# Optimization experiments

Hardware: AMD Instinct MI355X
Metric: run time of the kernel (lower is better)

Reference implementation:

```python
import jax, jax.numpy as jnp
import numpy as np

K = 49        # k_neighbors
EPS = 1e-5    # BatchNorm2d eps


def setup_inputs() -> dict:
    key = jax.random.key(0)
    ks = jax.random.split(key, 2)
    B, C, M, O = 64, 64, 32, 128
    X = jax.random.normal(ks[0], (B, C, M, M), dtype=jnp.float32)
    # conv1x1 weight (kaiming fan_out) flattened to (O, C); bias init 0
    W = jax.random.normal(ks[1], (O, C), dtype=jnp.float32) * (2.0 / O) ** 0.5
    b = jnp.zeros((O,), jnp.float32)
    gamma = jnp.ones((O,), jnp.float32)
    beta = jnp.zeros((O,), jnp.float32)
    run_mean = jnp.zeros((O,), jnp.float32)
    run_var = jnp.ones((O,), jnp.float32)
    return dict(X=X, W=W, b=b, gamma=gamma, beta=beta,
                run_mean=run_mean, run_var=run_var)


def _knn_aggregate(x):
    """x: (N, C) node features -> D^{-1/2} A D^{-1/2} x for the kNN graph."""
    N = x.shape[0]
    sq = jnp.sum(x * x, axis=1)
    d2 = sq[:, None] + sq[None, :] - 2.0 * (x @ x.T)
    dist = jnp.sqrt(jnp.maximum(d2, 0.0))              # torch.cdist (p=2)
    i = jnp.arange(N)
    dist = dist.at[i, i].set(jnp.inf)                  # fill_diagonal_(inf)
    _, knn = jax.lax.top_k(-dist, K)                   # (N, K) nearest indices
    # topk indices are distinct -> every row degree == K, and the column
    # normalizer uses the col node's row degree (also K), so
    # D^{-1/2} A D^{-1/2} x == mean of gathered neighbors.
    nb = x[knn]                                        # (N, K, C) gather
    return nb.sum(axis=1) / K


def reference(X, W, b, gamma, beta, run_mean, run_var):
    B, C, M, _ = X.shape
    N = M * M
    x = X.reshape(B, C, N).transpose(0, 2, 1)          # (B, N, C) nodes
    Z = jax.vmap(_knn_aggregate)(x)                    # (B, N, C) sparse GCN agg
    # 1x1 conv over the (M, M) grid == per-node linear map
    Fg = jnp.einsum('oc,bnc->bon', W, Z) + b[None, :, None]   # (B, O, N)
    Fg = jax.nn.relu(Fg)
    # BatchNorm2d with running stats (eval mode); Dropout2d is identity in eval
    inv = jax.lax.rsqrt(run_var + EPS)
    Fg = gamma[None, :, None] * (Fg - run_mean[None, :, None]) * inv[None, :, None] + beta[None, :, None]
    return Fg.mean(axis=2)                             # AdaptiveAvgPool2d(1) -> (B, O)
```

## Files before the change

kernel.cpp:

```cpp
#include <hip/hip_runtime.h>
#include <stdint.h>

#define BATCH 64
#define CDIM  64
#define NPTS  1024
#define ODIM  128
#define KNN   49
#define KNNP  52
#define BNEPS 1e-5f

typedef __attribute__((ext_vector_type(8))) short bf16x8;
typedef __attribute__((ext_vector_type(4))) float f32x4;

__device__ __forceinline__ int mbcnt64(unsigned long long m) {
    return __builtin_amdgcn_mbcnt_hi((uint32_t)(m >> 32),
           __builtin_amdgcn_mbcnt_lo((uint32_t)m, 0));
}

#define O_XF   0
#define SZ_XF  (BATCH*64*2*64*8*4)
#define O_SQ   (O_XF + SZ_XF)
#define SZ_SQ  (BATCH*NPTS*4)
#define O_KNN  (O_SQ + SZ_SQ)
#define SZ_KNN (BATCH*NPTS*KNNP*4)
#define O_Z    (O_KNN + SZ_KNN)
#define SZ_Z   (BATCH*NPTS*CDIM*4)
#define WS_NEED ((size_t)(O_Z + SZ_Z))

__global__ void gcn_init(const float* __restrict__ gamma, const float* __restrict__ beta,
                         const float* __restrict__ rmean, const float* __restrict__ rvar,
                         float* __restrict__ out) {
    int i = blockIdx.x * 256 + threadIdx.x;
    if (i < BATCH * ODIM) {
        int o = i & (ODIM - 1);
        out[i] = beta[o] - gamma[o] * rmean[o] * rsqrtf(rvar[o] + BNEPS);
    }
}

__global__ __launch_bounds__(256) void k0_split(const float* __restrict__ X,
                                                uint32_t* __restrict__ XF,
                                                float* __restrict__ sq,
                                                const float* __restrict__ gamma,
                                                const float* __restrict__ beta,
                                                const float* __restrict__ rmean,
                                                const float* __restrict__ rvar,
                                                float* __restrict__ out) {
    if (blockIdx.x < 32) {
        int i = blockIdx.x * 256 + threadIdx.x;
        int o = i & (ODIM - 1);
        out[i] = beta[o] - gamma[o] * rmean[o] * rsqrtf(rvar[o] + BNEPS);
    }
    const int b    = blockIdx.x >> 4;
    const int t16  = (blockIdx.x & 15) * 4 + (threadIdx.x >> 6);
    const int lane = threadIdx.x & 63;
    const int n    = t16 * 16 + (lane & 15);
    const int cg   = lane >> 4;
    const float* Xb = X + (size_t)b * CDIM * NPTS;
    float s = 0.f;
    for (int ks = 0; ks < 2; ks++) {
        uint32_t hi[4], lo[4];
#pragma unroll
        for (int dj = 0; dj < 4; dj++) {
            uint32_t hw[2], lw[2];
#pragma unroll
            for (int e = 0; e < 2; e++) {
                int c = ks * 32 + cg * 8 + dj * 2 + e;
                float x = Xb[(size_t)c * NPTS + n];
                s += x * x;
                uint32_t u  = __float_as_uint(x);
                uint32_t hr = (u + 0x7FFFu + ((u >> 16) & 1u)) >> 16;
                float    hf = __uint_as_float(hr << 16);
                uint32_t ul = __float_as_uint(x - hf);
                uint32_t lr = (ul + 0x7FFFu + ((ul >> 16) & 1u)) >> 16;
                hw[e] = hr; lw[e] = lr;
            }
            hi[dj] = hw[0] | (hw[1] << 16);
            lo[dj] = lw[0] | (lw[1] << 16);
        }
        size_t entry = ((size_t)(b * 64 + t16) * 2 + ks) * 64 + lane;
        uint32_t* p = XF + entry * 8;
        *(uint4*)p       = make_uint4(hi[0], hi[1], hi[2], hi[3]);
        *(uint4*)(p + 4) = make_uint4(lo[0], lo[1], lo[2], lo[3]);
    }
    s += __shfl_xor(s, 16, 64);
    s += __shfl_xor(s, 32, 64);
    if (lane < 16) sq[b * NPTS + n] = s;
}

__global__ __launch_bounds__(512, 6) void k1_gram_select(const uint32_t* __restrict__ XF,
                                                         const float* __restrict__ sq,
                                                         int* __restrict__ knn) {
    __shared__ uint32_t s_pk[8 * 1024];
    const int b    = blockIdx.x >> 6;
    const int rt   = blockIdx.x & 63;
    const int wave = threadIdx.x >> 6, lane = threadIdx.x & 63;
    const int q = lane >> 4, l15 = lane & 15;

    bf16x8 ahi[2], alo[2];
#pragma unroll
    for (int ks = 0; ks < 2; ks++) {
        const uint32_t* p = XF + (((size_t)(b * 64 + rt) * 2 + ks) * 64 + lane) * 8;
        ahi[ks] = *(const bf16x8*)p;
        alo[ks] = *(const bf16x8*)(p + 4);
    }
    const float* sqb = sq + b * NPTS;

#pragma unroll
    for (int tt = 0; tt < 8; tt++) {
        const int t16 = wave * 8 + tt;
        f32x4 acc = {0.f, 0.f, 0.f, 0.f};
#pragma unroll
        for (int ks = 0; ks < 2; ks++) {
            const uint32_t* p = XF + (((size_t)(b * 64 + t16) * 2 + ks) * 64 + lane) * 8;
            bf16x8 bhi = *(const bf16x8*)p;
            bf16x8 blo = *(const bf16x8*)(p + 4);
            acc = __builtin_amdgcn_mfma_f32_16x16x32_bf16(ahi[ks], bhi, acc, 0, 0, 0);
            acc = __builtin_amdgcn_mfma_f32_16x16x32_bf16(alo[ks], bhi, acc, 0, 0, 0);
            acc = __builtin_amdgcn_mfma_f32_16x16x32_bf16(ahi[ks], blo, acc, 0, 0, 0);
        }
        const int col  = t16 * 16 + l15;
        const float sqv = sqb[col];
        uint32_t k16[4];
#pragma unroll
        for (int i = 0; i < 4; i++) {
            int row = q * 4 + i;
            float d = fmaf(-2.f, acc[i], sqv);
            if (col == rt * 16 + row) d = __uint_as_float(0x7F800000u);
            uint32_t u = __float_as_uint(d);
            uint32_t key = ((int)u < 0) ? ~u : (u | 0x80000000u);
            k16[i] = key >> 16;
        }
        const int p0 = 2 * q, p1 = 2 * q + 1;
        s_pk[p0 * 1024 + (col ^ ((p0 & 3) << 3))] = k16[0] | (k16[1] << 16);
        s_pk[p1 * 1024 + (col ^ ((p1 & 3) << 3))] = k16[2] | (k16[3] << 16);
    }
    __syncthreads();

    uint32_t k0r[16], k1r[16];
    {
        const int sw = (wave & 3) << 3;
#pragma unroll
        for (int tt = 0; tt < 16; tt++) {
            uint32_t pk = s_pk[wave * 1024 + ((tt * 64 + lane) ^ sw)];
            k0r[tt] = pk & 0xFFFFu;
            k1r[tt] = pk >> 16;
        }
    }

    uint32_t lo0, hi0, lo1, hi1;
    {
        uint32_t lm0 = k0r[0], lm1 = k1r[0];
#pragma unroll
        for (int tt = 1; tt < 16; tt++) {
            lm0 = k0r[tt] < lm0 ? k0r[tt] : lm0;
            lm1 = k1r[tt] < lm1 ? k1r[tt] : lm1;
        }
        uint32_t g0 = lm0, m0 = lm0, g1 = lm1, m1 = lm1;
#pragma unroll
        for (int off = 1; off < 64; off <<= 1) {
            uint32_t a0 = (uint32_t)__shfl_xor((int)g0, off, 64);
            uint32_t b0 = (uint32_t)__shfl_xor((int)m0, off, 64);
            uint32_t a1 = (uint32_t)__shfl_xor((int)g1, off, 64);
            uint32_t b1 = (uint32_t)__shfl_xor((int)m1, off, 64);
            g0 = a0 < g0 ? a0 : g0;  m0 = b0 > m0 ? b0 : m0;
            g1 = a1 < g1 ? a1 : g1;  m1 = b1 > m1 ? b1 : m1;
        }
        lo0 = g0; hi0 = m0;
        lo1 = g1; hi1 = m1;
    }

    for (int it = 0; it < 16; it++) {
        bool a0 = lo0 < hi0, a1 = lo1 < hi1;
        if (!a0 && !a1) break;
        uint32_t mid0 = (lo0 + hi0) >> 1;
        uint32_t mid1 = (lo1 + hi1) >> 1;
        int cnt0 = 0, cnt1 = 0;
#pragma unroll
        for (int tt = 0; tt < 16; tt++) {
            cnt0 += __popcll(__ballot(k0r[tt] <= mid0));
            cnt1 += __popcll(__ballot(k1r[tt] <= mid1));
        }
        if (a0) { if (cnt0 >= KNN) hi0 = mid0; else lo0 = mid0 + 1; }
        if (a1) { if (cnt1 >= KNN) hi1 = mid1; else lo1 = mid1 + 1; }
    }

#pragma unroll
    for (int r = 0; r < 2; r++) {
        const int row = wave * 2 + r;
        const uint32_t vstar = r ? lo1 : lo0;
        const uint32_t* k = r ? k1r : k0r;
        int total_lt = 0;
#pragma unroll
        for (int tt = 0; tt < 16; tt++)
            total_lt += __popcll(__ballot(k[tt] < vstar));
        int base_lt = 0, base_eq = total_lt;
        int* kout = knn + ((size_t)b * NPTS + rt * 16 + row) * KNNP;
#pragma unroll
        for (int tt = 0; tt < 16; tt++) {
            bool islt = k[tt] < vstar;
            bool iseq = k[tt] == vstar;
            unsigned long long mlt = __ballot(islt);
            unsigned long long meq = __ballot(iseq);
            if (mlt | meq) {
                int pos = islt ? (base_lt + mbcnt64(mlt)) : (base_eq + mbcnt64(meq));
                if (islt || (iseq && pos < KNN)) kout[pos] = tt * 64 + lane;
            }
            base_lt += __popcll(mlt);
            base_eq += __popcll(meq);
        }
    }
}

__global__ __launch_bounds__(256) void k2a_aggregate(const float* __restrict__ X,
                                                     const int* __restrict__ knn,
                                                     float* __restrict__ z) {
    __shared__ float XT[16 * 1024];
    const int b = blockIdx.x >> 3, cg = (blockIdx.x >> 1) & 3, half = blockIdx.x & 1;
    const int t = threadIdx.x;
    const float* Xb = X + ((size_t)b * CDIM + cg * 16) * NPTS;
#pragma unroll
    for (int nn = 0; nn < 4; nn++) {
        int n = nn * 256 + t;
#pragma unroll
        for (int g = 0; g < 4; g++) {
            float4 v;
            v.x = Xb[(size_t)(4 * g + 0) * NPTS + n];
            v.y = Xb[(size_t)(4 * g + 1) * NPTS + n];
            v.z = Xb[(size_t)(4 * g + 2) * NPTS + n];
            v.w = Xb[(size_t)(4 * g + 3) * NPTS + n];
            int qp = g ^ ((n >> 1) & 3);
            *(float4*)&XT[n * 16 + qp * 4] = v;
        }
    }
    __syncthreads();
    const int wave = t >> 6, lane = t & 63;
    const int rl = lane >> 2, g = lane & 3;
    for (int rr = 0; rr < 8; rr++) {
        const int row = half * 512 + wave * 128 + rr * 16 + rl;
        const int* kr = knn + ((size_t)b * NPTS + row) * KNNP;
        int4 j[13];
#pragma unroll
        for (int c = 0; c < 13; c++) j[c] = *(const int4*)&kr[c * 4];
        float4 s = {0.f, 0.f, 0.f, 0.f};
#pragma unroll
        for (int c = 0; c < 12; c++) {
            int js[4] = {j[c].x, j[c].y, j[c].z, j[c].w};
#pragma unroll
            for (int e = 0; e < 4; e++) {
                int jj = js[e];
                float4 v = *(const float4*)&XT[jj * 16 + ((g ^ ((jj >> 1) & 3)) << 2)];
                s.x += v.x; s.y += v.y; s.z += v.z; s.w += v.w;
            }
        }
        {
            int jj = j[12].x;
            float4 v = *(const float4*)&XT[jj * 16 + ((g ^ ((jj >> 1) & 3)) << 2)];
            s.x += v.x; s.y += v.y; s.z += v.z; s.w += v.w;
        }
        *(float4*)&z[((size_t)b * NPTS + row) * CDIM + cg * 16 + g * 4] = s;
    }
}

__global__ __launch_bounds__(256) void k2b_gemm(const float* __restrict__ z,
                                                const float* __restrict__ W,
                                                const float* __restrict__ bias,
                                                const float* __restrict__ gamma,
                                                const float* __restrict__ rvar,
                                                float* __restrict__ out) {
    __shared__ __align__(16) float s_zz[128 * 64];
    __shared__ float s_red[2][256];
    const int b = blockIdx.x >> 3, nq = blockIdx.x & 7;
    const int t = threadIdx.x;
    const float* zb = z + ((size_t)b * NPTS + nq * 128) * CDIM;
#pragma unroll
    for (int qq = 0; qq < 8; qq++) {
        int e = qq * 256 + t;
        *(float4*)&s_zz[e * 4] = *(const float4*)&zb[e * 4];
    }
    __syncthreads();
    const int o2 = t & 63, h = t >> 6;
    float4 w0[16], w1[16];
#pragma unroll
    for (int c4 = 0; c4 < 16; c4++) {
        w0[c4] = *(const float4*)&W[(size_t)o2 * CDIM + c4 * 4];
        w1[c4] = *(const float4*)&W[(size_t)(o2 + 64) * CDIM + c4 * 4];
    }
    const float b0 = bias[o2], b1 = bias[o2 + 64];
    float r0 = 0.f, r1 = 0.f;
    for (int r = 0; r < 32; r++) {
        const float* zr = &s_zz[(h * 32 + r) * 64];
        float a0 = 0.f, a1 = 0.f;
#pragma unroll
        for (int c4 = 0; c4 < 16; c4++) {
            float4 zv = *(const float4*)&zr[c4 * 4];
            a0 += w0[c4].x * zv.x + w0[c4].y * zv.y + w0[c4].z * zv.z + w0[c4].w * zv.w;
            a1 += w1[c4].x * zv.x + w1[c4].y * zv.y + w1[c4].z * zv.z + w1[c4].w * zv.w;
        }
        r0 += fmaxf(a0 * (1.f / KNN) + b0, 0.f);
        r1 += fmaxf(a1 * (1.f / KNN) + b1, 0.f);
    }
    s_red[0][t] = r0; s_red[1][t] = r1;
    __syncthreads();
    if (t < 128) {
        const int oo = t & 63, which = t >> 6;
        const int o = which * 64 + oo;
        float sum = s_red[which][oo] + s_red[which][64 + oo] +
                    s_red[which][128 + oo] + s_red[which][192 + oo];
        float scale = gamma[o] * rsqrtf(rvar[o] + BNEPS) * (1.f / NPTS);
        atomicAdd(&out[b * ODIM + o], sum * scale);
    }
}

#define RTILE 8
#define APAD  1028
#define WPAD  132
#define POOLF (64 * WPAD)

__global__ __launch_bounds__(256) void gcn_main(
    const float* __restrict__ X, const float* __restrict__ W,
    const float* __restrict__ bias, const float* __restrict__ gamma,
    const float* __restrict__ rvar, float* __restrict__ out)
{
    __shared__ __align__(16) float s_pool[POOLF];
    __shared__ __align__(16) float s_fstage[4][APAD];
    __shared__ int   s_knn[RTILE][KNN];
    __shared__ float s_z[RTILE][CDIM];

    const int t = threadIdx.x;
    const int b = blockIdx.x >> 7;
    const int rtile = blockIdx.x & 127;
    const int r0 = rtile * RTILE;
    const float* Xb = X + (size_t)b * CDIM * NPTS;

    float acc[RTILE][4];
    float sqv[4];
#pragma unroll
    for (int r = 0; r < RTILE; r++)
#pragma unroll
        for (int u = 0; u < 4; u++) acc[r][u] = 0.f;
#pragma unroll
    for (int u = 0; u < 4; u++) sqv[u] = 0.f;

    for (int ch = 0; ch < 16; ch++) {
        const int c0 = ch * 4;
#pragma unroll
        for (int cc = 0; cc < 4; cc++) {
            float4 v = *(const float4*)(Xb + (size_t)(c0 + cc) * NPTS + 4 * t);
            *(float4*)&s_fstage[cc][4 * t] = v;
        }
        __syncthreads();
#pragma unroll
        for (int cc = 0; cc < 4; cc++) {
            float4 bv4 = *(const float4*)&s_fstage[cc][4 * t];
            float bv[4] = {bv4.x, bv4.y, bv4.z, bv4.w};
#pragma unroll
            for (int u = 0; u < 4; u++) sqv[u] += bv[u] * bv[u];
            const float* arow = Xb + (size_t)(c0 + cc) * NPTS + r0;
            float4 a0 = *(const float4*)(arow);
            float4 a1 = *(const float4*)(arow + 4);
            float av[8] = {a0.x, a0.y, a0.z, a0.w, a1.x, a1.y, a1.z, a1.w};
#pragma unroll
            for (int r = 0; r < RTILE; r++)
#pragma unroll
                for (int u = 0; u < 4; u++) acc[r][u] += av[r] * bv[u];
        }
        __syncthreads();
    }

    float* s_dist = s_pool;
#pragma unroll
    for (int r = 0; r < RTILE; r++) {
        const int rG = r0 + r;
        float d[4];
#pragma unroll
        for (int u = 0; u < 4; u++) {
            float dd = sqv[u] - 2.f * acc[r][u];
            d[u] = (4 * t + u == rG) ? __uint_as_float(0x7F800000u) : dd;
        }
        *(float4*)&s_dist[r * NPTS + 4 * t] = make_float4(d[0], d[1], d[2], d[3]);
    }
    __syncthreads();

    const int wave = t >> 6, lane = t & 63;
    const unsigned long long ltmask = (1ull << lane) - 1ull;
    for (int rr = 0; rr < 2; rr++) {
        const int row = wave * 2 + rr;
        unsigned key[16];
#pragma unroll
        for (int tt = 0; tt < 16; tt++) {
            unsigned u = __float_as_uint(s_dist[row * NPTS + tt * 64 + lane]);
            key[tt] = (u & 0x80000000u) ? ~u : (u | 0x80000000u);
        }
        unsigned lo = 0u, hi = 0xFFFFFFFFu;
        while (lo < hi) {
            unsigned mid = lo + ((hi - lo) >> 1);
            int cnt = 0;
#pragma unroll
            for (int tt = 0; tt < 16; tt++)
                cnt += __popcll(__ballot(key[tt] <= mid));
            if (cnt >= KNN) hi = mid; else lo = mid + 1;
        }
        const unsigned v49 = lo;
        int cntless = 0;
#pragma unroll
        for (int tt = 0; tt < 16; tt++)
            cntless += __popcll(__ballot(key[tt] < v49));
        const int need = KNN - cntless;
        int base = 0, eqtaken = 0;
#pragma unroll
        for (int tt = 0; tt < 16; tt++) {
            bool islt = key[tt] < v49;
            bool iseq = key[tt] == v49;
            unsigned long long meq = __ballot(iseq);
            int eqrank = eqtaken + __popcll(meq & ltmask);
            bool sel = islt || (iseq && (eqrank < need));
            unsigned long long msel = __ballot(sel);
            if (sel) {
                int pos = base + __popcll(msel & ltmask);
                s_knn[row][pos] = tt * 64 + lane;
            }
            base    += __popcll(msel);
            eqtaken += __popcll(meq);
        }
    }
    __syncthreads();

    float* astage = s_pool;
    float* s_redf = (float*)s_fstage;
    const int ar = t >> 5, acc8 = (t & 31) >> 2, ks = t & 3;
    for (int c0 = 0; c0 < CDIM; c0 += 8) {
#pragma unroll
        for (int qq = 0; qq < 8; qq++) {
            int if4 = qq * 256 + t;
            int cc = if4 >> 8, j4 = if4 & 255;
            float4 v = *(const float4*)(Xb + (size_t)(c0 + cc) * NPTS + 4 * j4);
            *(float4*)&astage[cc * APAD + 4 * j4] = v;
        }
        __syncthreads();
        float partial = 0.f;
        for (int k = ks; k < KNN; k += 4)
            partial += astage[acc8 * APAD + s_knn[ar][k]];
        s_redf[t] = partial;
        __syncthreads();
        if (t < 64) {
            int r = t >> 3, cc = t & 7;
            int bi = r * 32 + cc * 4;
            s_z[r][c0 + cc] = s_redf[bi] + s_redf[bi + 1] + s_redf[bi + 2] + s_redf[bi + 3];
        }
        __syncthreads();
    }

    float* wt = s_pool;
#pragma unroll 4
    for (int qq = 0; qq < 32; qq++) {
        int e = qq * 256 + t;
        int o = e >> 6, c = e & 63;
        wt[c * WPAD + o] = W[e];
    }
    __syncthreads();
    const int o = t & 127, rg = t >> 7;
    float facc[4] = {0.f, 0.f, 0.f, 0.f};
    for (int c = 0; c < CDIM; c += 4) {
        float w0 = wt[(c + 0) * WPAD + o], w1 = wt[(c + 1) * WPAD + o];
        float w2 = wt[(c + 2) * WPAD + o], w3 = wt[(c + 3) * WPAD + o];
#pragma unroll
        for (int qq = 0; qq < 4; qq++) {
            float4 zv = *(const float4*)&s_z[rg * 4 + qq][c];
            facc[qq] += w0 * zv.x + w1 * zv.y + w2 * zv.z + w3 * zv.w;
        }
    }
    const float bo = bias[o];
    float rsum = 0.f;
#pragma unroll
    for (int qq = 0; qq < 4; qq++) {
        float f = facc[qq] * (1.f / KNN) + bo;
        rsum += fmaxf(f, 0.f);
    }
    s_redf[t] = rsum;
    __syncthreads();
    if (t < 128) {
        float scale = gamma[t] * rsqrtf(rvar[t] + BNEPS) * (1.f / NPTS);
        atomicAdd(&out[b * ODIM + t], (s_redf[t] + s_redf[t + 128]) * scale);
    }
}

extern "C" void kernel_launch(void* const* d_in, const int* in_sizes, int n_in,
                              void* d_out, int out_size, void* d_ws, size_t ws_size,
                              hipStream_t stream) {
    const float* X     = (const float*)d_in[0];
    const float* W     = (const float*)d_in[1];
    const float* bias  = (const float*)d_in[2];
    const float* gamma = (const float*)d_in[3];
    const float* beta  = (const float*)d_in[4];
    const float* rmean = (const float*)d_in[5];
    const float* rvar  = (const float*)d_in[6];
    float* out = (float*)d_out;

    if (ws_size >= WS_NEED) {
        uint8_t* ws = (uint8_t*)d_ws;
        uint32_t* XF  = (uint32_t*)(ws + O_XF);
        float*    sqw = (float*)(ws + O_SQ);
        int*      knn = (int*)(ws + O_KNN);
        float*    zw  = (float*)(ws + O_Z);
        k0_split<<<BATCH * 16, 256, 0, stream>>>(X, XF, sqw, gamma, beta, rmean, rvar, out);
        k1_gram_select<<<BATCH * 64, 512, 0, stream>>>(XF, sqw, knn);
        k2a_aggregate<<<BATCH * 8, 256, 0, stream>>>(X, knn, zw);
        k2b_gemm<<<BATCH * 8, 256, 0, stream>>>(zw, W, bias, gamma, rvar, out);
    } else {
        gcn_init<<<(BATCH * ODIM + 255) / 256, 256, 0, stream>>>(gamma, beta, rmean, rvar, out);
        gcn_main<<<BATCH * (NPTS / RTILE), 256, 0, stream>>>(X, W, bias, gamma, rvar, out);
    }
}
```

Baseline: 273.0 us.

## Fuse kNN aggregation with conv GEMM and stage kNN indices in LDS

Merges the aggregate and GEMM kernels into one kernel per (batch, 128-row) tile. The aggregated features stay in shared memory instead of going through a global Z buffer. Each block loops over eight channel groups, transposing X into LDS and gathering neighbors, then runs the per-node linear map with a rotated layout to avoid bank conflicts. The select kernel now writes the kNN indices to LDS and stores them to global with coalesced int4 writes, and its occupancy hint is dropped. In exchange, X is reloaded per 128-row tile across eight passes with more barriers, and the new kernel has fewer output channels per thread.

```diff
diff --git a/kernel.cpp b/kernel.cpp
--- a/kernel.cpp
+++ b/kernel.cpp
@@ -23,9 +23,7 @@
 #define SZ_SQ  (BATCH*NPTS*4)
 #define O_KNN  (O_SQ + SZ_SQ)
 #define SZ_KNN (BATCH*NPTS*KNNP*4)
-#define O_Z    (O_KNN + SZ_KNN)
-#define SZ_Z   (BATCH*NPTS*CDIM*4)
-#define WS_NEED ((size_t)(O_Z + SZ_Z))
+#define WS_NEED ((size_t)(O_KNN + SZ_KNN))
 
 __global__ void gcn_init(const float* __restrict__ gamma, const float* __restrict__ beta,
                          const float* __restrict__ rmean, const float* __restrict__ rvar,
@@ -87,14 +85,15 @@
     if (lane < 16) sq[b * NPTS + n] = s;
 }
 
-__global__ __launch_bounds__(512, 6) void k1_gram_select(const uint32_t* __restrict__ XF,
-                                                         const float* __restrict__ sq,
-                                                         int* __restrict__ knn) {
+__global__ __launch_bounds__(512) void k1_gram_select(const uint32_t* __restrict__ XF,
+                                                      const float* __restrict__ sq,
+                                                      int* __restrict__ knn) {
     __shared__ uint32_t s_pk[8 * 1024];
     const int b    = blockIdx.x >> 6;
     const int rt   = blockIdx.x & 63;
     const int wave = threadIdx.x >> 6, lane = threadIdx.x & 63;
     const int q = lane >> 4, l15 = lane & 15;
+    int* eknn = (int*)s_pk;
 
     bf16x8 ahi[2], alo[2];
 #pragma unroll
@@ -146,6 +145,8 @@
             k1r[tt] = pk >> 16;
         }
     }
+    __syncthreads();
+    if (threadIdx.x < 208) *(int4*)&eknn[threadIdx.x * 4] = make_int4(0, 0, 0, 0);
 
     uint32_t lo0, hi0, lo1, hi1;
     {
@@ -194,7 +195,6 @@
         for (int tt = 0; tt < 16; tt++)
             total_lt += __popcll(__ballot(k[tt] < vstar));
         int base_lt = 0, base_eq = total_lt;
-        int* kout = knn + ((size_t)b * NPTS + rt * 16 + row) * KNNP;
 #pragma unroll
         for (int tt = 0; tt < 16; tt++) {
             bool islt = k[tt] < vstar;
@@ -203,111 +203,109 @@
             unsigned long long meq = __ballot(iseq);
             if (mlt | meq) {
                 int pos = islt ? (base_lt + mbcnt64(mlt)) : (base_eq + mbcnt64(meq));
-                if (islt || (iseq && pos < KNN)) kout[pos] = tt * 64 + lane;
+                if (islt || (iseq && pos < KNN)) eknn[row * KNNP + pos] = tt * 64 + lane;
             }
             base_lt += __popcll(mlt);
             base_eq += __popcll(meq);
         }
     }
-}
-
-__global__ __launch_bounds__(256) void k2a_aggregate(const float* __restrict__ X,
-                                                     const int* __restrict__ knn,
-                                                     float* __restrict__ z) {
-    __shared__ float XT[16 * 1024];
-    const int b = blockIdx.x >> 3, cg = (blockIdx.x >> 1) & 3, half = blockIdx.x & 1;
-    const int t = threadIdx.x;
-    const float* Xb = X + ((size_t)b * CDIM + cg * 16) * NPTS;
-#pragma unroll
-    for (int nn = 0; nn < 4; nn++) {
-        int n = nn * 256 + t;
-#pragma unroll
-        for (int g = 0; g < 4; g++) {
-            float4 v;
-            v.x = Xb[(size_t)(4 * g + 0) * NPTS + n];
-            v.y = Xb[(size_t)(4 * g + 1) * NPTS + n];
-            v.z = Xb[(size_t)(4 * g + 2) * NPTS + n];
-            v.w = Xb[(size_t)(4 * g + 3) * NPTS + n];
-            int qp = g ^ ((n >> 1) & 3);
-            *(float4*)&XT[n * 16 + qp * 4] = v;
-        }
-    }
-    __syncthreads();
-    const int wave = t >> 6, lane = t & 63;
-    const int rl = lane >> 2, g = lane & 3;
-    for (int rr = 0; rr < 8; rr++) {
-        const int row = half * 512 + wave * 128 + rr * 16 + rl;
-        const int* kr = knn + ((size_t)b * NPTS + row) * KNNP;
-        int4 j[13];
-#pragma unroll
-        for (int c = 0; c < 13; c++) j[c] = *(const int4*)&kr[c * 4];
-        float4 s = {0.f, 0.f, 0.f, 0.f};
-#pragma unroll
-        for (int c = 0; c < 12; c++) {
-            int js[4] = {j[c].x, j[c].y, j[c].z, j[c].w};
-#pragma unroll
-            for (int e = 0; e < 4; e++) {
-                int jj = js[e];
-                float4 v = *(const float4*)&XT[jj * 16 + ((g ^ ((jj >> 1) & 3)) << 2)];
-                s.x += v.x; s.y += v.y; s.z += v.z; s.w += v.w;
-            }
-        }
-        {
-            int jj = j[12].x;
-            float4 v = *(const float4*)&XT[jj * 16 + ((g ^ ((jj >> 1) & 3)) << 2)];
-            s.x += v.x; s.y += v.y; s.z += v.z; s.w += v.w;
-        }
-        *(float4*)&z[((size_t)b * NPTS + row) * CDIM + cg * 16 + g * 4] = s;
-    }
-}
-
-__global__ __launch_bounds__(256) void k2b_gemm(const float* __restrict__ z,
+    __syncthreads();
+    {
+        const int t = threadIdx.x;
+        int* kbase = knn + ((size_t)b * NPTS + rt * 16) * KNNP;
+        if (t < 208) *(int4*)&kbase[t * 4] = *(const int4*)&eknn[t * 4];
+    }
+}
+
+__global__ __launch_bounds__(256) void k2_fused(const float* __restrict__ X,
+                                                const int* __restrict__ knn,
                                                 const float* __restrict__ W,
                                                 const float* __restrict__ bias,
                                                 const float* __restrict__ gamma,
                                                 const float* __restrict__ rvar,
                                                 float* __restrict__ out) {
-    __shared__ __align__(16) float s_zz[128 * 64];
-    __shared__ float s_red[2][256];
+    __shared__ __align__(16) float XT8[8 * 1024];
+    __shared__ float s_red[256];
     const int b = blockIdx.x >> 3, nq = blockIdx.x & 7;
     const int t = threadIdx.x;
-    const float* zb = z + ((size_t)b * NPTS + nq * 128) * CDIM;
-#pragma unroll
-    for (int qq = 0; qq < 8; qq++) {
-        int e = qq * 256 + t;
-        *(float4*)&s_zz[e * 4] = *(const float4*)&zb[e * 4];
-    }
-    __syncthreads();
-    const int o2 = t & 63, h = t >> 6;
-    float4 w0[16], w1[16];
-#pragma unroll
-    for (int c4 = 0; c4 < 16; c4++) {
-        w0[c4] = *(const float4*)&W[(size_t)o2 * CDIM + c4 * 4];
-        w1[c4] = *(const float4*)&W[(size_t)(o2 + 64) * CDIM + c4 * 4];
-    }
-    const float b0 = bias[o2], b1 = bias[o2 + 64];
-    float r0 = 0.f, r1 = 0.f;
-    for (int r = 0; r < 32; r++) {
-        const float* zr = &s_zz[(h * 32 + r) * 64];
-        float a0 = 0.f, a1 = 0.f;
+    const int rl = t >> 1, gg = t & 1;
+    const int row = nq * 128 + rl;
+    const int* kr = knn + ((size_t)b * NPTS + row) * KNNP;
+    int4 j[13];
+#pragma unroll
+    for (int c = 0; c < 13; c++) j[c] = *(const int4*)&kr[c * 4];
+
+    float4 zacc[8];
+    for (int cg8 = 0; cg8 < 8; cg8++) {
+        __syncthreads();
+        const float* Xc = X + ((size_t)b * CDIM + cg8 * 8) * NPTS;
+#pragma unroll
+        for (int k4 = 0; k4 < 4; k4++) {
+            int n = k4 * 256 + t;
+#pragma unroll
+            for (int g2 = 0; g2 < 2; g2++) {
+                float4 v;
+                v.x = Xc[(size_t)(g2 * 4 + 0) * NPTS + n];
+                v.y = Xc[(size_t)(g2 * 4 + 1) * NPTS + n];
+                v.z = Xc[(size_t)(g2 * 4 + 2) * NPTS + n];
+                v.w = Xc[(size_t)(g2 * 4 + 3) * NPTS + n];
+                int sl = (g2 ^ (n & 1)) << 2;
+                *(float4*)&XT8[n * 8 + sl] = v;
+            }
+        }
+        __syncthreads();
+        float4 s = {0.f, 0.f, 0.f, 0.f};
+#pragma unroll
+        for (int c = 0; c < 12; c++) {
+            int js[4] = {j[c].x, j[c].y, j[c].z, j[c].w};
+#pragma unroll
+            for (int e = 0; e < 4; e++) {
+                int jj = js[e];
+                float4 v = *(const float4*)&XT8[jj * 8 + ((gg ^ (jj & 1)) << 2)];
+                s.x += v.x; s.y += v.y; s.z += v.z; s.w += v.w;
+            }
+        }
+        {
+            int jj = j[12].x;
+            float4 v = *(const float4*)&XT8[jj * 8 + ((gg ^ (jj & 1)) << 2)];
+            s.x += v.x; s.y += v.y; s.z += v.z; s.w += v.w;
+        }
+        zacc[cg8] = s;
+    }
+    __syncthreads();
+    float* ZT = XT8;
+#pragma unroll
+    for (int cg8 = 0; cg8 < 8; cg8++) {
+        int colr = ((cg8 * 8 + gg * 4) + (rl & 15) * 4) & 63;
+        *(float4*)&ZT[rl * 64 + colr] = zacc[cg8];
+    }
+    __syncthreads();
+
+    const int o = t & 127, h = t >> 7;
+    float4 wv[16];
+#pragma unroll
+    for (int c4 = 0; c4 < 16; c4++)
+        wv[c4] = *(const float4*)&W[(size_t)o * CDIM + c4 * 4];
+    const float bo = bias[o];
+    float rsum = 0.f;
+    for (int r = 0; r < 64; r++) {
+        const int zr = h * 64 + r;
+        const float* zrow = &ZT[zr * 64];
+        const int rot = (zr & 15) * 4;
+        float a = 0.f;
 #pragma unroll
         for (int c4 = 0; c4 < 16; c4++) {
-            float4 zv = *(const float4*)&zr[c4 * 4];
-            a0 += w0[c4].x * zv.x + w0[c4].y * zv.y + w0[c4].z * zv.z + w0[c4].w * zv.w;
-            a1 += w1[c4].x * zv.x + w1[c4].y * zv.y + w1[c4].z * zv.z + w1[c4].w * zv.w;
-        }
-        r0 += fmaxf(a0 * (1.f / KNN) + b0, 0.f);
-        r1 += fmaxf(a1 * (1.f / KNN) + b1, 0.f);
-    }
-    s_red[0][t] = r0; s_red[1][t] = r1;
+            float4 zv = *(const float4*)&zrow[(c4 * 4 + rot) & 63];
+            a += wv[c4].x * zv.x + wv[c4].y * zv.y + wv[c4].z * zv.z + wv[c4].w * zv.w;
+        }
+        rsum += fmaxf(a * (1.f / KNN) + bo, 0.f);
+    }
+    s_red[t] = rsum;
     __syncthreads();
     if (t < 128) {
-        const int oo = t & 63, which = t >> 6;
-        const int o = which * 64 + oo;
-        float sum = s_red[which][oo] + s_red[which][64 + oo] +
-                    s_red[which][128 + oo] + s_red[which][192 + oo];
-        float scale = gamma[o] * rsqrtf(rvar[o] + BNEPS) * (1.f / NPTS);
-        atomicAdd(&out[b * ODIM + o], sum * scale);
+        float sum = s_red[t] + s_red[t + 128];
+        float scale = gamma[t] * rsqrtf(rvar[t] + BNEPS) * (1.f / NPTS);
+        atomicAdd(&out[b * ODIM + t], sum * scale);
     }
 }
 
@@ -501,11 +499,9 @@
         uint32_t* XF  = (uint32_t*)(ws + O_XF);
         float*    sqw = (float*)(ws + O_SQ);
         int*      knn = (int*)(ws + O_KNN);
-        float*    zw  = (float*)(ws + O_Z);
         k0_split<<<BATCH * 16, 256, 0, stream>>>(X, XF, sqw, gamma, beta, rmean, rvar, out);
         k1_gram_select<<<BATCH * 64, 512, 0, stream>>>(XF, sqw, knn);
-        k2a_aggregate<<<BATCH * 8, 256, 0, stream>>>(X, knn, zw);
-        k2b_gemm<<<BATCH * 8, 256, 0, stream>>>(zw, W, bias, gamma, rvar, out);
+        k2_fused<<<BATCH * 8, 256, 0, stream>>>(X, knn, W, bias, gamma, rvar, out);
     } else {
         gcn_init<<<(BATCH * ODIM + 255) / 256, 256, 0, stream>>>(gamma, beta, rmean, rvar, out);
         gcn_main<<<BATCH * (NPTS / RTILE), 256, 0, stream>>>(X, W, bias, gamma, rvar, out);
```

Result: no change. 278.4 us (+2.0%).
